# Kernel optimization log

Hardware: AMD Instinct MI355X
Metric: run time of the kernel (lower is better)

Reference implementation:

```python
import jax, jax.numpy as jnp
import numpy as np


def _gcn_conv(x, edge_index, edge_weight, W, b, n_nodes):
    # PyG GCNConv with normalize=True: add self-loops (weight 1), symmetric norm,
    # transform then aggregate: out[col] += norm * (x @ W)[row], plus bias.
    row = jnp.concatenate([edge_index[0], jnp.arange(n_nodes)])
    col = jnp.concatenate([edge_index[1], jnp.arange(n_nodes)])
    w = jnp.concatenate([edge_weight, jnp.ones((n_nodes,), x.dtype)])
    deg = jax.ops.segment_sum(w, col, num_segments=n_nodes)
    dinv = jnp.where(deg > 0, jax.lax.rsqrt(jnp.maximum(deg, 1e-12)), 0.0)
    norm = dinv[row] * w * dinv[col]            # [E+N]
    h = x @ W                                   # [N, out]
    msg = h[row] * norm[:, None]                # [E+N, out]
    out = jax.ops.segment_sum(msg, col, num_segments=n_nodes)
    return out + b


def setup_inputs() -> dict:
    key = jax.random.key(0)
    ks = jax.random.split(key, 6)
    N, E, F_IN, H, C = 50000, 800000, 512, 128, 40
    features = jax.random.normal(ks[0], (N, F_IN), jnp.float32)
    edge_index = jax.random.randint(ks[1], (2, E), 0, N, jnp.int64)
    edge_weight = jax.random.uniform(ks[2], (E,), jnp.float32)
    W1 = jax.random.normal(ks[3], (F_IN, H), jnp.float32) * 0.05
    b1 = jnp.zeros((H,), jnp.float32)
    W2 = jax.random.normal(ks[4], (H, C), jnp.float32) * 0.05
    b2 = jnp.zeros((C,), jnp.float32)
    return {"features": features, "edge_index": edge_index, "edge_weight": edge_weight,
            "W1": W1, "b1": b1, "W2": W2, "b2": b2}


def reference(features, edge_index, edge_weight, W1, b1, W2, b2):
    n_nodes = features.shape[0]
    x = _gcn_conv(features, edge_index, edge_weight, W1, b1, n_nodes)
    x = jax.nn.relu(x)
    # F.dropout(training=self.training): identity in eval mode
    x = _gcn_conv(x, edge_index, edge_weight, W2, b2, n_nodes)
    return jax.nn.log_softmax(x, axis=1)
```

## Files before the change

### kernel.cpp

```cpp
#include <hip/hip_runtime.h>
#include <math.h>

#define FIN  512
#define HDIM 128
#define CDIM 40
#define CPAD 48
#define CAP  64

typedef __attribute__((ext_vector_type(8))) short shortx8;
typedef __attribute__((ext_vector_type(4))) float f32x4;
typedef __attribute__((ext_vector_type(2))) float floatx2;

__device__ inline unsigned short f2bf(float x) {
    unsigned u = __builtin_bit_cast(unsigned, x);
    unsigned r = u + 0x7fffu + ((u >> 16) & 1u);
    return (unsigned short)(r >> 16);
}
__device__ inline float bfu(unsigned short v) { return __builtin_bit_cast(float, (unsigned)v << 16); }
__device__ inline float bfhi(unsigned u) { return __builtin_bit_cast(float, u & 0xffff0000u); }
__device__ inline unsigned char f2fp8(float x) {
    return (unsigned char)(__builtin_amdgcn_cvt_pk_fp8_f32(x, x, 0, false) & 0xff);
}
__device__ inline floatx2 fp8x2_dec(unsigned short v) {
    return __builtin_amdgcn_cvt_pk_f32_fp8((int)(unsigned)v, false);
}

#define PREPB 280
__global__ void k_prep(const float* __restrict__ W1, const float* __restrict__ W2,
                       unsigned short* __restrict__ W1T, unsigned short* __restrict__ W2T,
                       unsigned long long* __restrict__ cursor, int n) {
    const int b = blockIdx.x;
    if (b < PREPB) {
        const int i = b * 256 + (int)threadIdx.x;
        if (i < FIN * HDIM) {
            const int k = i >> 7, nn = i & 127;
            W1T[nn * FIN + k] = f2bf(W1[i]);
        } else {
            const int j = i - FIN * HDIM;
            const int nn = j >> 7, k = j & 127;
            W2T[j] = (nn < CDIM) ? f2bf(W2[k * CDIM + nn]) : (unsigned short)0;
        }
    } else {
        const int i = (b - PREPB) * 256 + (int)threadIdx.x;
        if (i < n) cursor[i] = 0ULL;
    }
}

#define G1_LDA 72
__global__ __launch_bounds__(512) void k_fillg1(
    const float* __restrict__ A, const unsigned short* __restrict__ W1T,
    unsigned char* __restrict__ h1f8, int M, int g1b,
    const int* __restrict__ row, const int* __restrict__ col,
    const float* __restrict__ w,
    unsigned long long* __restrict__ cursor, unsigned* __restrict__ bkt, int E) {
    __shared__ short As[128 * G1_LDA];
    __shared__ short Bs[128 * G1_LDA];
    const int tid = threadIdx.x;

    if ((int)blockIdx.x >= g1b) {
        const int e = ((int)blockIdx.x - g1b) * 512 + tid;
        if (e >= E) return;
        const int c = col[e];
        const float we = w[e];
        const unsigned long long wfix = (unsigned long long)(we * 4294967296.0f);
        const unsigned long long old = atomicAdd(&cursor[c], (1ULL << 40) | wfix);
        const int p = (int)(old >> 40);
        const unsigned wb = (__builtin_bit_cast(unsigned, we) + 0x8000u) >> 16;
        if (p < CAP) bkt[(size_t)c * CAP + p] = (wb << 16) | (unsigned)row[e];
        return;
    }

    const int wave = tid >> 6;
    const int lane = tid & 63;
    const int quad = lane >> 4;
    const int mr   = lane & 15;
    const int m0w  = (wave >> 1) * 32;
    const int n0w  = (wave & 1) * 64;
    const int m0b  = blockIdx.x * 128;

    const int srow  = tid >> 2;
    const int spart = tid & 3;

    f32x4 acc[2][4];
#pragma unroll
    for (int i = 0; i < 2; i++)
#pragma unroll
        for (int j = 0; j < 4; j++) acc[i][j] = (f32x4)0.f;

    const int grow = m0b + srow;
    const bool arow_ok = grow < M;
    const float* ap = A + (size_t)grow * FIN + spart * 16;
    const unsigned short* bp = W1T + (size_t)srow * FIN + spart * 16;

    for (int k0 = 0; k0 < FIN; k0 += 64) {
        {
            float4 v0 = make_float4(0.f, 0.f, 0.f, 0.f), v1 = v0, v2 = v0, v3 = v0;
            if (arow_ok) {
                v0 = *(const float4*)(ap + k0);
                v1 = *(const float4*)(ap + k0 + 4);
                v2 = *(const float4*)(ap + k0 + 8);
                v3 = *(const float4*)(ap + k0 + 12);
            }
            shortx8 p0, p1;
            p0[0] = (short)f2bf(v0.x); p0[1] = (short)f2bf(v0.y);
            p0[2] = (short)f2bf(v0.z); p0[3] = (short)f2bf(v0.w);
            p0[4] = (short)f2bf(v1.x); p0[5] = (short)f2bf(v1.y);
            p0[6] = (short)f2bf(v1.z); p0[7] = (short)f2bf(v1.w);
            p1[0] = (short)f2bf(v2.x); p1[1] = (short)f2bf(v2.y);
            p1[2] = (short)f2bf(v2.z); p1[3] = (short)f2bf(v2.w);
            p1[4] = (short)f2bf(v3.x); p1[5] = (short)f2bf(v3.y);
            p1[6] = (short)f2bf(v3.z); p1[7] = (short)f2bf(v3.w);
            *(shortx8*)&As[srow * G1_LDA + spart * 16]     = p0;
            *(shortx8*)&As[srow * G1_LDA + spart * 16 + 8] = p1;
        }
        *(shortx8*)&Bs[srow * G1_LDA + spart * 16]     = *(const shortx8*)(bp + k0);
        *(shortx8*)&Bs[srow * G1_LDA + spart * 16 + 8] = *(const shortx8*)(bp + k0 + 8);
        __syncthreads();

#pragma unroll
        for (int kk = 0; kk < 2; kk++) {
            shortx8 af[2], bfr[4];
#pragma unroll
            for (int mt = 0; mt < 2; mt++)
                af[mt] = *(shortx8*)&As[(m0w + mt * 16 + mr) * G1_LDA + kk * 32 + quad * 8];
#pragma unroll
            for (int nt = 0; nt < 4; nt++)
                bfr[nt] = *(shortx8*)&Bs[(n0w + nt * 16 + mr) * G1_LDA + kk * 32 + quad * 8];
#pragma unroll
            for (int mt = 0; mt < 2; mt++)
#pragma unroll
                for (int nt = 0; nt < 4; nt++)
                    acc[mt][nt] = __builtin_amdgcn_mfma_f32_16x16x32_bf16(
                        af[mt], bfr[nt], acc[mt][nt], 0, 0, 0);
        }
        __syncthreads();
    }
#pragma unroll
    for (int mt = 0; mt < 2; mt++)
#pragma unroll
        for (int r = 0; r < 4; r++) {
            const int om = m0b + m0w + mt * 16 + quad * 4 + r;
            if (om < M) {
#pragma unroll
                for (int nt = 0; nt < 4; nt++)
                    h1f8[(size_t)om * HDIM + n0w + nt * 16 + mr] = f2fp8(acc[mt][nt][r]);
            }
        }
}

__global__ void k_dinv(const unsigned long long* __restrict__ cursor,
                       int* __restrict__ cnt, float* __restrict__ dinv, int n) {
    const int i = blockIdx.x * 256 + threadIdx.x;
    if (i < n) {
        const unsigned long long p = cursor[i];
        cnt[i] = min((int)(p >> 40), CAP);
        dinv[i] = rsqrtf(1.0f + (float)(p & ((1ULL << 40) - 1)) * 2.3283064365386963e-10f);
    }
}

#define W2LD 130
__global__ __launch_bounds__(256) void k_g1g2(
    const int* __restrict__ cnt_arr, const float* __restrict__ dinv,
    const unsigned* __restrict__ bkt,
    const unsigned char* __restrict__ h1f8,
    const float* __restrict__ b1,
    const unsigned short* __restrict__ W2T,
    unsigned short* __restrict__ h2, int n_nodes) {
    __shared__ unsigned short W2s[CPAD * W2LD];
    __shared__ unsigned short Xs[4 * 128];
    const int tid  = threadIdx.x;
    const int wave = tid >> 6;
    const int lane = tid & 63;
    const int loff = lane * 2;

    for (int i = tid; i < CPAD * (HDIM / 8); i += 256) {
        const int r = i >> 4, j = (i & 15) * 8;
        *(shortx8*)&W2s[r * W2LD + j] = *(const shortx8*)(W2T + r * HDIM + j);
    }
    __syncthreads();

    const int node = blockIdx.x * 4 + wave;
    if (node >= n_nodes) return;
    const int cnt = cnt_arr[node];
    const float dl = dinv[node];
    const char* bb = (const char*)bkt + (unsigned)node * (CAP * 4u);
    float a0 = 0.f, a1 = 0.f, c0 = 0.f, c1 = 0.f;
    int s = 0;
    for (; s + 8 <= cnt; s += 8) {
        const uint4 qa = *(const uint4*)(bb + (unsigned)s * 4u);
        const uint4 qb = *(const uint4*)(bb + (unsigned)s * 4u + 16u);
        const float w0 = bfhi(qa.x) * dinv[qa.x & 0xffffu];
        const float w1 = bfhi(qa.y) * dinv[qa.y & 0xffffu];
        const float w2 = bfhi(qa.z) * dinv[qa.z & 0xffffu];
        const float w3 = bfhi(qa.w) * dinv[qa.w & 0xffffu];
        const float w4 = bfhi(qb.x) * dinv[qb.x & 0xffffu];
        const float w5 = bfhi(qb.y) * dinv[qb.y & 0xffffu];
        const float w6 = bfhi(qb.z) * dinv[qb.z & 0xffffu];
        const float w7 = bfhi(qb.w) * dinv[qb.w & 0xffffu];
        const unsigned short v0 = *(const unsigned short*)(h1f8 + (qa.x & 0xffffu) * 128u + (unsigned)loff);
        const unsigned short v1 = *(const unsigned short*)(h1f8 + (qa.y & 0xffffu) * 128u + (unsigned)loff);
        const unsigned short v2 = *(const unsigned short*)(h1f8 + (qa.z & 0xffffu) * 128u + (unsigned)loff);
        const unsigned short v3 = *(const unsigned short*)(h1f8 + (qa.w & 0xffffu) * 128u + (unsigned)loff);
        const unsigned short v4 = *(const unsigned short*)(h1f8 + (qb.x & 0xffffu) * 128u + (unsigned)loff);
        const unsigned short v5 = *(const unsigned short*)(h1f8 + (qb.y & 0xffffu) * 128u + (unsigned)loff);
        const unsigned short v6 = *(const unsigned short*)(h1f8 + (qb.z & 0xffffu) * 128u + (unsigned)loff);
        const unsigned short v7 = *(const unsigned short*)(h1f8 + (qb.w & 0xffffu) * 128u + (unsigned)loff);
        const floatx2 f0 = fp8x2_dec(v0), f1 = fp8x2_dec(v1), f2 = fp8x2_dec(v2), f3 = fp8x2_dec(v3);
        const floatx2 f4 = fp8x2_dec(v4), f5 = fp8x2_dec(v5), f6 = fp8x2_dec(v6), f7 = fp8x2_dec(v7);
        a0 += w0 * f0.x + w1 * f1.x + w2 * f2.x + w3 * f3.x;
        a1 += w0 * f0.y + w1 * f1.y + w2 * f2.y + w3 * f3.y;
        c0 += w4 * f4.x + w5 * f5.x + w6 * f6.x + w7 * f7.x;
        c1 += w4 * f4.y + w5 * f5.y + w6 * f6.y + w7 * f7.y;
    }
    for (; s + 4 <= cnt; s += 4) {
        const uint4 qa = *(const uint4*)(bb + (unsigned)s * 4u);
        const float w0 = bfhi(qa.x) * dinv[qa.x & 0xffffu];
        const float w1 = bfhi(qa.y) * dinv[qa.y & 0xffffu];
        const float w2 = bfhi(qa.z) * dinv[qa.z & 0xffffu];
        const float w3 = bfhi(qa.w) * dinv[qa.w & 0xffffu];
        const unsigned short v0 = *(const unsigned short*)(h1f8 + (qa.x & 0xffffu) * 128u + (unsigned)loff);
        const unsigned short v1 = *(const unsigned short*)(h1f8 + (qa.y & 0xffffu) * 128u + (unsigned)loff);
        const unsigned short v2 = *(const unsigned short*)(h1f8 + (qa.z & 0xffffu) * 128u + (unsigned)loff);
        const unsigned short v3 = *(const unsigned short*)(h1f8 + (qa.w & 0xffffu) * 128u + (unsigned)loff);
        const floatx2 f0 = fp8x2_dec(v0), f1 = fp8x2_dec(v1), f2 = fp8x2_dec(v2), f3 = fp8x2_dec(v3);
        a0 += w0 * f0.x + w1 * f1.x + w2 * f2.x + w3 * f3.x;
        a1 += w0 * f0.y + w1 * f1.y + w2 * f2.y + w3 * f3.y;
    }
    for (; s < cnt; s++) {
        const unsigned p = *(const unsigned*)(bb + (unsigned)s * 4u);
        const float w0 = bfhi(p) * dinv[p & 0xffffu];
        const unsigned short v = *(const unsigned short*)(h1f8 + (p & 0xffffu) * 128u + (unsigned)loff);
        const floatx2 f = fp8x2_dec(v);
        a0 += w0 * f.x;
        a1 += w0 * f.y;
    }
    a0 += c0; a1 += c1;
    const unsigned short vs = *(const unsigned short*)(h1f8 + (unsigned)node * 128u + (unsigned)loff);
    const floatx2 fs = fp8x2_dec(vs);
    a0 = fmaxf(dl * (a0 + dl * fs.x) + b1[loff], 0.f);
    a1 = fmaxf(dl * (a1 + dl * fs.y) + b1[loff + 1], 0.f);
    *(unsigned*)&Xs[wave * 128 + loff] = (unsigned)f2bf(a0) | ((unsigned)f2bf(a1) << 16);

    const int quad = lane >> 4;
    const int mr   = lane & 15;
    f32x4 acc2[3];
#pragma unroll
    for (int nt = 0; nt < 3; nt++) acc2[nt] = (f32x4)0.f;
#pragma unroll
    for (int kc = 0; kc < 4; kc++) {
        shortx8 af = (shortx8)0;
        if (mr == 0) af = *(const shortx8*)&Xs[wave * 128 + kc * 32 + quad * 8];
#pragma unroll
        for (int nt = 0; nt < 3; nt++) {
            const shortx8 bfr = *(const shortx8*)&W2s[(nt * 16 + mr) * W2LD + kc * 32 + quad * 8];
            acc2[nt] = __builtin_amdgcn_mfma_f32_16x16x32_bf16(af, bfr, acc2[nt], 0, 0, 0);
        }
    }
    if (lane < 16) {
        h2[(size_t)node * 32 + lane]      = f2bf(dl * acc2[0][0]);
        h2[(size_t)node * 32 + 16 + lane] = f2bf(dl * acc2[1][0]);
        if (lane < 8)
            h2[(size_t)n_nodes * 32 + (size_t)node * 8 + lane] = f2bf(dl * acc2[2][0]);
    }
}

__global__ __launch_bounds__(256) void k_gather2(
    const int* __restrict__ cnt_arr, const float* __restrict__ dinv,
    const unsigned* __restrict__ bkt,
    const unsigned short* __restrict__ h2,
    const float* __restrict__ b2,
    float* __restrict__ out, int n_nodes) {
    const int node = blockIdx.x * 4 + (threadIdx.x >> 6);
    const int lane = threadIdx.x & 63;
    if (node >= n_nodes) return;
    const bool act = lane < CDIM;
    const int cnt = cnt_arr[node];
    const float dl = dinv[node];
    const char* bb = (const char*)bkt + (unsigned)node * (CAP * 4u);
    const char* h2c = (const char*)h2;
    const unsigned strB = (lane < 32) ? 64u : 16u;
    const unsigned cb   = (lane < 32) ? (unsigned)lane * 2u
                                      : (unsigned)n_nodes * 64u + (unsigned)(lane - 32) * 2u;
    float acc = 0.f, accb = 0.f;
    int s = 0;
    for (; s + 4 <= cnt; s += 4) {
        const uint4 q = *(const uint4*)(bb + (unsigned)s * 4u);
        if (act) {
            const unsigned short u0 = *(const unsigned short*)(h2c + (q.x & 0xffffu) * strB + cb);
            const unsigned short u1 = *(const unsigned short*)(h2c + (q.y & 0xffffu) * strB + cb);
            const unsigned short u2 = *(const unsigned short*)(h2c + (q.z & 0xffffu) * strB + cb);
            const unsigned short u3 = *(const unsigned short*)(h2c + (q.w & 0xffffu) * strB + cb);
            acc  += bfhi(q.x) * bfu(u0) + bfhi(q.y) * bfu(u1);
            accb += bfhi(q.z) * bfu(u2) + bfhi(q.w) * bfu(u3);
        }
    }
    for (; s < cnt; s++) {
        const unsigned p = *(const unsigned*)(bb + (unsigned)s * 4u);
        if (act) acc += bfhi(p) * bfu(*(const unsigned short*)(h2c + (p & 0xffffu) * strB + cb));
    }
    acc += accb;
    if (act) {
        const unsigned short us = *(const unsigned short*)(h2c + (unsigned)node * strB + cb);
        acc = dl * (acc + bfu(us)) + b2[lane];
    }
    float m = act ? acc : -INFINITY;
#pragma unroll
    for (int off = 32; off; off >>= 1) m = fmaxf(m, __shfl_xor(m, off));
    float se = act ? expf(acc - m) : 0.f;
#pragma unroll
    for (int off = 32; off; off >>= 1) se += __shfl_xor(se, off);
    if (act) out[(size_t)node * CDIM + lane] = acc - m - logf(se);
}

extern "C" void kernel_launch(void* const* d_in, const int* in_sizes, int n_in,
                              void* d_out, int out_size, void* d_ws, size_t ws_size,
                              hipStream_t stream) {
    const float* features = (const float*)d_in[0];
    const int*   eidx     = (const int*)d_in[1];
    const float* ew       = (const float*)d_in[2];
    const float* W1       = (const float*)d_in[3];
    const float* b1       = (const float*)d_in[4];
    const float* W2       = (const float*)d_in[5];
    const float* b2       = (const float*)d_in[6];
    float* out = (float*)d_out;

    const int Nn = in_sizes[0] / FIN;
    const int E  = in_sizes[2];
    const int* row = eidx;
    const int* col = eidx + E;

    char* ws = (char*)d_ws;
    size_t off = 0;
    auto alloc = [&](size_t bytes) { void* p = ws + off; off += (bytes + 255) & ~(size_t)255; return p; };
    unsigned long long* cursor = (unsigned long long*)alloc((size_t)Nn * 8);
    int*      cnt          = (int*)     alloc((size_t)Nn * 4);
    float*    dinv         = (float*)   alloc((size_t)Nn * 4);
    unsigned* bkt          = (unsigned*)alloc((size_t)Nn * CAP * 4);
    unsigned short* W1T    = (unsigned short*)alloc((size_t)FIN * HDIM * 2);
    unsigned short* W2T    = (unsigned short*)alloc((size_t)CPAD * HDIM * 2);
    unsigned char*  h1f8   = (unsigned char*) alloc((size_t)Nn * HDIM);
    unsigned short* h2     = (unsigned short*)alloc((size_t)Nn * 40 * 2);

    const int eblocks = (E + 511) / 512;
    const int g1b = (Nn + 127) / 128;

    k_prep<<<PREPB + (Nn + 255) / 256, 256, 0, stream>>>(W1, W2, W1T, W2T, cursor, Nn);
    k_fillg1<<<g1b + eblocks, 512, 0, stream>>>(features, W1T, h1f8, Nn, g1b,
                                                row, col, ew, cursor, bkt, E);
    k_dinv<<<(Nn + 255) / 256, 256, 0, stream>>>(cursor, cnt, dinv, Nn);
    k_g1g2<<<(Nn + 3) / 4, 256, 0, stream>>>(cnt, dinv, bkt, h1f8, b1, W2T, h2, Nn);
    k_gather2<<<(Nn + 3) / 4, 256, 0, stream>>>(cnt, dinv, bkt, h2, b2, out, Nn);
}
```

Baseline: 297.6 us.

## Shrink GEMM block tile to 64 rows and prefetch next K-slice into registers

The fused GEMM+bucket-fill kernel now uses 256-thread blocks with a 64x128 output tile instead of 512 threads and 128x128, which doubles the number of GEMM blocks. The next K-slice of the feature matrix and W1T is loaded into registers right after the barrier, so the global loads overlap the MFMA work. The trailing __syncthreads is replaced by an LDS wait plus a raw barrier. This adds register pressure and makes each block reload W1T more often relative to the rows it computes, but it should hide global latency and give better occupancy.

```diff
diff --git a/kernel.cpp b/kernel.cpp
--- a/kernel.cpp
+++ b/kernel.cpp
@@ -47,18 +47,18 @@
 }
 
 #define G1_LDA 72
-__global__ __launch_bounds__(512) void k_fillg1(
+__global__ __launch_bounds__(256) void k_fillg1(
     const float* __restrict__ A, const unsigned short* __restrict__ W1T,
     unsigned char* __restrict__ h1f8, int M, int g1b,
     const int* __restrict__ row, const int* __restrict__ col,
     const float* __restrict__ w,
     unsigned long long* __restrict__ cursor, unsigned* __restrict__ bkt, int E) {
-    __shared__ short As[128 * G1_LDA];
+    __shared__ short As[64 * G1_LDA];
     __shared__ short Bs[128 * G1_LDA];
     const int tid = threadIdx.x;
 
     if ((int)blockIdx.x >= g1b) {
-        const int e = ((int)blockIdx.x - g1b) * 512 + tid;
+        const int e = ((int)blockIdx.x - g1b) * 256 + tid;
         if (e >= E) return;
         const int c = col[e];
         const float we = w[e];
@@ -74,12 +74,12 @@
     const int lane = tid & 63;
     const int quad = lane >> 4;
     const int mr   = lane & 15;
-    const int m0w  = (wave >> 1) * 32;
-    const int n0w  = (wave & 1) * 64;
-    const int m0b  = blockIdx.x * 128;
-
-    const int srow  = tid >> 2;
-    const int spart = tid & 3;
+    const int m0w  = (wave & 1) * 32;
+    const int n0w  = (wave >> 1) * 64;
+    const int m0b  = blockIdx.x * 64;
+
+    const int srowA = tid >> 2, spartA = tid & 3;
+    const int srowB = tid >> 1, spartB = tid & 1;
 
     f32x4 acc[2][4];
 #pragma unroll
@@ -87,35 +87,54 @@
 #pragma unroll
         for (int j = 0; j < 4; j++) acc[i][j] = (f32x4)0.f;
 
-    const int grow = m0b + srow;
-    const bool arow_ok = grow < M;
-    const float* ap = A + (size_t)grow * FIN + spart * 16;
-    const unsigned short* bp = W1T + (size_t)srow * FIN + spart * 16;
+    const int growA = m0b + srowA;
+    const bool okA = growA < M;
+    const float* ap = A + (size_t)growA * FIN + spartA * 16;
+    const unsigned short* bp = W1T + (size_t)srowB * FIN + spartB * 32;
+
+    const float4 z4 = make_float4(0.f, 0.f, 0.f, 0.f);
+    float4 pa0, pa1, pa2, pa3;
+    shortx8 pb0, pb1, pb2, pb3;
+    pa0 = okA ? *(const float4*)(ap + 0)  : z4;
+    pa1 = okA ? *(const float4*)(ap + 4)  : z4;
+    pa2 = okA ? *(const float4*)(ap + 8)  : z4;
+    pa3 = okA ? *(const float4*)(ap + 12) : z4;
+    pb0 = *(const shortx8*)(bp + 0);
+    pb1 = *(const shortx8*)(bp + 8);
+    pb2 = *(const shortx8*)(bp + 16);
+    pb3 = *(const shortx8*)(bp + 24);
 
     for (int k0 = 0; k0 < FIN; k0 += 64) {
         {
-            float4 v0 = make_float4(0.f, 0.f, 0.f, 0.f), v1 = v0, v2 = v0, v3 = v0;
-            if (arow_ok) {
-                v0 = *(const float4*)(ap + k0);
-                v1 = *(const float4*)(ap + k0 + 4);
-                v2 = *(const float4*)(ap + k0 + 8);
-                v3 = *(const float4*)(ap + k0 + 12);
-            }
-            shortx8 p0, p1;
-            p0[0] = (short)f2bf(v0.x); p0[1] = (short)f2bf(v0.y);
-            p0[2] = (short)f2bf(v0.z); p0[3] = (short)f2bf(v0.w);
-            p0[4] = (short)f2bf(v1.x); p0[5] = (short)f2bf(v1.y);
-            p0[6] = (short)f2bf(v1.z); p0[7] = (short)f2bf(v1.w);
-            p1[0] = (short)f2bf(v2.x); p1[1] = (short)f2bf(v2.y);
-            p1[2] = (short)f2bf(v2.z); p1[3] = (short)f2bf(v2.w);
-            p1[4] = (short)f2bf(v3.x); p1[5] = (short)f2bf(v3.y);
-            p1[6] = (short)f2bf(v3.z); p1[7] = (short)f2bf(v3.w);
-            *(shortx8*)&As[srow * G1_LDA + spart * 16]     = p0;
-            *(shortx8*)&As[srow * G1_LDA + spart * 16 + 8] = p1;
-        }
-        *(shortx8*)&Bs[srow * G1_LDA + spart * 16]     = *(const shortx8*)(bp + k0);
-        *(shortx8*)&Bs[srow * G1_LDA + spart * 16 + 8] = *(const shortx8*)(bp + k0 + 8);
+            shortx8 q0, q1;
+            q0[0] = (short)f2bf(pa0.x); q0[1] = (short)f2bf(pa0.y);
+            q0[2] = (short)f2bf(pa0.z); q0[3] = (short)f2bf(pa0.w);
+            q0[4] = (short)f2bf(pa1.x); q0[5] = (short)f2bf(pa1.y);
+            q0[6] = (short)f2bf(pa1.z); q0[7] = (short)f2bf(pa1.w);
+            q1[0] = (short)f2bf(pa2.x); q1[1] = (short)f2bf(pa2.y);
+            q1[2] = (short)f2bf(pa2.z); q1[3] = (short)f2bf(pa2.w);
+            q1[4] = (short)f2bf(pa3.x); q1[5] = (short)f2bf(pa3.y);
+            q1[6] = (short)f2bf(pa3.z); q1[7] = (short)f2bf(pa3.w);
+            *(shortx8*)&As[srowA * G1_LDA + spartA * 16]      = q0;
+            *(shortx8*)&As[srowA * G1_LDA + spartA * 16 + 8]  = q1;
+            *(shortx8*)&Bs[srowB * G1_LDA + spartB * 32]      = pb0;
+            *(shortx8*)&Bs[srowB * G1_LDA + spartB * 32 + 8]  = pb1;
+            *(shortx8*)&Bs[srowB * G1_LDA + spartB * 32 + 16] = pb2;
+            *(shortx8*)&Bs[srowB * G1_LDA + spartB * 32 + 24] = pb3;
+        }
         __syncthreads();
+
+        const int kn = k0 + 64;
+        if (kn < FIN) {
+            pa0 = okA ? *(const float4*)(ap + kn)      : z4;
+            pa1 = okA ? *(const float4*)(ap + kn + 4)  : z4;
+            pa2 = okA ? *(const float4*)(ap + kn + 8)  : z4;
+            pa3 = okA ? *(const float4*)(ap + kn + 12) : z4;
+            pb0 = *(const shortx8*)(bp + kn);
+            pb1 = *(const shortx8*)(bp + kn + 8);
+            pb2 = *(const shortx8*)(bp + kn + 16);
+            pb3 = *(const shortx8*)(bp + kn + 24);
+        }
 
 #pragma unroll
         for (int kk = 0; kk < 2; kk++) {
@@ -133,7 +152,8 @@
                     acc[mt][nt] = __builtin_amdgcn_mfma_f32_16x16x32_bf16(
                         af[mt], bfr[nt], acc[mt][nt], 0, 0, 0);
         }
-        __syncthreads();
+        asm volatile("s_waitcnt lgkmcnt(0)" ::: "memory");
+        __builtin_amdgcn_s_barrier();
     }
 #pragma unroll
     for (int mt = 0; mt < 2; mt++)
@@ -341,11 +361,11 @@
     unsigned char*  h1f8   = (unsigned char*) alloc((size_t)Nn * HDIM);
     unsigned short* h2     = (unsigned short*)alloc((size_t)Nn * 40 * 2);
 
-    const int eblocks = (E + 511) / 512;
-    const int g1b = (Nn + 127) / 128;
+    const int eblocks = (E + 255) / 256;
+    const int g1b = (Nn + 63) / 64;
 
     k_prep<<<PREPB + (Nn + 255) / 256, 256, 0, stream>>>(W1, W2, W1T, W2T, cursor, Nn);
-    k_fillg1<<<g1b + eblocks, 512, 0, stream>>>(features, W1T, h1f8, Nn, g1b,
+    k_fillg1<<<g1b + eblocks, 256, 0, stream>>>(features, W1T, h1f8, Nn, g1b,
                                                 row, col, ew, cursor, bkt, E);
     k_dinv<<<(Nn + 255) / 256, 256, 0, stream>>>(cursor, cnt, dinv, Nn);
     k_g1g2<<<(Nn + 3) / 4, 256, 0, stream>>>(cnt, dinv, bkt, h1f8, b1, W2T, h2, Nn);
```

After: 321.1 us. 1.08x slower.
